# Optimization experiments

Measured on AMD Instinct MI355X. Metric: run time of the kernel, lower is better.

Reference implementation:

```python
import jax, jax.numpy as jnp
import numpy as np

B, N, M, D, R, K = 4, 4096, 4096, 256, 64, 16
EPS = 1e-5

def layernorm(x, g, b):
    m = jnp.mean(x, axis=-1, keepdims=True)
    v = jnp.var(x, axis=-1, keepdims=True)
    return (x - m) * jax.lax.rsqrt(v + EPS) * g + b

def signed_softmax(x):
    # sign(x) * softmax(|x|) along last axis
    return jnp.sign(x) * jax.nn.softmax(jnp.abs(x), axis=-1)

def unit(v):
    return v / (jnp.linalg.norm(v, axis=-1, keepdims=True) + 1e-6)

def bgather(x, idx):
    # x: [B, Msrc, ...], idx: [B, Ndst, K] -> [B, Ndst, K, ...]
    return jax.vmap(lambda xv, iv: xv[iv])(x, idx)

def topk_abs(scores, k):
    # top-k by absolute score, keep signed values
    _, idx = jax.lax.top_k(jnp.abs(scores), k)
    w = jnp.take_along_axis(scores, idx, axis=-1)
    return w, idx

def lr_bilinear_scores(src_val, dst_val, U, V):
    # scores[b, n_dst, m_src] = (dst V) . (src U) / sqrt(rank)
    sp = jnp.einsum('bmd,dr->bmr', src_val, U)
    dp = jnp.einsum('bnd,dr->bnr', dst_val, V)
    return jnp.einsum('bnr,bmr->bnm', dp, sp) / jnp.sqrt(jnp.asarray(U.shape[1], src_val.dtype))

def sparse_transition(src_state, src_val, dst_val, U, V, k):
    scores = lr_bilinear_scores(src_val, dst_val, U, V)  # [B, Ndst, Msrc]
    w, idx = topk_abs(scores, k)                          # [B, Ndst, k]
    wts = signed_softmax(w) * jax.nn.softplus(bgather(src_state, idx))
    msgs = unit(bgather(src_val, idx))                    # direction-only messages
    dval = jnp.einsum('bnk,bnkd->bnd', wts, msgs)
    dstate = jnp.sum(wts, axis=-1)
    return dstate, dval

def sparse_propagation(val_norm, U, V, k):
    scores = lr_bilinear_scores(val_norm, val_norm, U, V)  # [B, N, N]
    w, idx = topk_abs(scores, k)
    wts = signed_softmax(w)  # state_weight_edges=False
    msgs = unit(bgather(val_norm, idx))
    dval = jnp.einsum('bnk,bnkd->bnd', wts, msgs)
    dstate = jnp.sum(wts, axis=-1)
    return dstate, dval

def apply_delta(state, val, dstate, dval, g, b):
    return signed_softmax(state + dstate), layernorm(val + dval, g, b)

def setup_inputs() -> dict:
    key = jax.random.key(0)
    ks = jax.random.split(key, 12)
    std = 0.02
    return {
        'b_state': jax.random.normal(ks[0], (B, M), jnp.float32),
        'b_val': jax.random.normal(ks[1], (B, M, D), jnp.float32),
        'init_state': jax.random.normal(ks[2], (N,), jnp.float32) * std,
        'init_val': jax.random.normal(ks[3], (N, D), jnp.float32) * std,
        'U_bk': jax.random.normal(ks[4], (D, R), jnp.float32) * std,
        'V_bk': jax.random.normal(ks[5], (D, R), jnp.float32) * std,
        'U_kb': jax.random.normal(ks[6], (D, R), jnp.float32) * std,
        'V_kb': jax.random.normal(ks[7], (D, R), jnp.float32) * std,
        'U_p': jax.random.normal(ks[8], (D, R), jnp.float32) * std,
        'V_p': jax.random.normal(ks[9], (D, R), jnp.float32) * std,
        'kn_g': jnp.ones((D,), jnp.float32), 'kn_b': jnp.zeros((D,), jnp.float32),
        'bn_g': jnp.ones((D,), jnp.float32), 'bn_b': jnp.zeros((D,), jnp.float32),
        'pn_g': jnp.ones((D,), jnp.float32), 'pn_b': jnp.zeros((D,), jnp.float32),
    }

def reference(b_state, b_val, init_state, init_val, U_bk, V_bk, U_kb, V_kb, U_p, V_p, kn_g, kn_b, bn_g, bn_b, pn_g, pn_b):
    Bsz = b_state.shape[0]
    # initialize_state
    k_state = signed_softmax(jnp.broadcast_to(init_state, (Bsz, init_state.shape[0])))
    k_val = layernorm(jnp.broadcast_to(init_val, (Bsz,) + init_val.shape), kn_g, kn_b)
    # route_from_b: B -> K sparse transition, residual + k_val_norm
    nk = layernorm(k_val, kn_g, kn_b)
    ds, dv = sparse_transition(b_state, b_val, nk, U_bk, V_bk, K)
    r_state, r_val = apply_delta(k_state, k_val, ds, dv, kn_g, kn_b)
    # propagate: 1 sparse propagation layer, residual + k_val_norm
    nv = layernorm(r_val, pn_g, pn_b)
    ds, dv = sparse_propagation(nv, U_p, V_p, K)
    p_state, p_val = apply_delta(r_state, r_val, ds, dv, kn_g, kn_b)
    # transition_to_b: K -> B delta (update_b=False)
    nk2 = layernorm(p_val, kn_g, kn_b)
    nb = layernorm(b_val, bn_g, bn_b)
    bds, bdv = sparse_transition(p_state, nk2, nb, U_kb, V_kb, K)
    return (r_state, r_val, p_state, p_val, bds, bdv)
```

## Files before the change

### kernel.cpp

```cpp
#include <hip/hip_runtime.h>
#include <hip/hip_bf16.h>

#define BB 4
#define NN 4096
#define DD 256
#define RR 64
#define KK 16
#define TM 16

typedef __attribute__((ext_vector_type(8))) short bf16x8;
typedef __attribute__((ext_vector_type(4))) float f32x4;

__device__ __forceinline__ void f32_split(float x, ushort* h, ushort* l){
  __hip_bfloat16 hb = __float2bfloat16(x);
  float hf = __bfloat162float(hb);
  __hip_bfloat16 lb = __float2bfloat16(x - hf);
  *h = *(ushort*)&hb; *l = *(ushort*)&lb;
}

__global__ void __launch_bounds__(1024) ssm_kernel(
    const float* __restrict__ xf, long xf_stride,
    const float* __restrict__ add, long add_stride,
    float* __restrict__ outf, long outf_stride)
{
  __shared__ float sm[32];
  int t = threadIdx.x;
  long b = blockIdx.x;
  float x[4]; float mx = 0.f;
  #pragma unroll
  for (int j=0;j<4;j++){
    int i = t + j*1024;
    float v = xf[b*xf_stride + i];
    if (add) v += add[b*add_stride + i];
    x[j]=v; mx = fmaxf(mx, fabsf(v));
  }
  #pragma unroll
  for (int o=1;o<64;o<<=1) mx = fmaxf(mx, __shfl_xor(mx,o,64));
  int wid = t>>6;
  if ((t&63)==0) sm[wid]=mx;
  __syncthreads();
  mx = sm[0];
  #pragma unroll
  for (int w=1;w<16;w++) mx = fmaxf(mx, sm[w]);
  float e[4]; float ssum=0.f;
  #pragma unroll
  for (int j=0;j<4;j++){ e[j]=expf(fabsf(x[j])-mx); ssum+=e[j]; }
  #pragma unroll
  for (int o=1;o<64;o<<=1) ssum += __shfl_xor(ssum,o,64);
  if ((t&63)==0) sm[16+wid]=ssum;
  __syncthreads();
  ssum = sm[16];
  #pragma unroll
  for (int w=1;w<16;w++) ssum += sm[16+w];
  float inv = 1.0f/ssum;
  #pragma unroll
  for (int j=0;j<4;j++){
    int i = t + j*1024;
    float sg = (x[j]>0.f)?1.f:((x[j]<0.f)?-1.f:0.f);
    outf[b*outf_stride + i] = sg*e[j]*inv;
  }
}

__global__ void __launch_bounds__(256) proj_ln_kernel(
    const float* __restrict__ src,
    const float* __restrict__ lg, const float* __restrict__ lb, int nln,
    const float* __restrict__ U, ushort* __restrict__ oUh, ushort* __restrict__ oUl, float scaleU,
    const float* __restrict__ V, ushort* __restrict__ oVh, ushort* __restrict__ oVl, float scaleV,
    float* __restrict__ nvout, float* __restrict__ nrmout)
{
  __shared__ float xs[TM][DD];
  __shared__ float ut[64*64];
  __shared__ float vt[64*64];
  int t = threadIdx.x;
  int wid = t>>6, lane = t&63;
  long row0 = (long)blockIdx.x*TM;

  float gv[4], bv[4];
  if (nln){
    #pragma unroll
    for (int u=0;u<4;u++){ int d=u*64+lane; gv[u]=lg[d]; bv[u]=lb[d]; }
  }
  for (int rr=0; rr<4; rr++){
    int r = wid*4 + rr;
    const float* srow = src + (row0 + r)*DD;
    float x[4];
    #pragma unroll
    for (int u=0;u<4;u++) x[u] = srow[u*64 + lane];
    for (int p=0;p<nln;p++){
      float s=0.f,q=0.f;
      #pragma unroll
      for (int u=0;u<4;u++){ s+=x[u]; q+=x[u]*x[u]; }
      #pragma unroll
      for (int o=1;o<64;o<<=1){ s+=__shfl_xor(s,o,64); q+=__shfl_xor(q,o,64); }
      float m = s*(1.f/DD), var = q*(1.f/DD)-m*m, rstd = rsqrtf(var+1e-5f);
      #pragma unroll
      for (int u=0;u<4;u++) x[u] = (x[u]-m)*rstd*gv[u]+bv[u];
    }
    if (nrmout){
      float ss=0.f;
      #pragma unroll
      for (int u=0;u<4;u++) ss += x[u]*x[u];
      #pragma unroll
      for (int o=1;o<64;o<<=1) ss += __shfl_xor(ss,o,64);
      if (lane==0) nrmout[row0 + r] = 1.f/(sqrtf(ss)+1e-6f);
    }
    if (nvout){
      #pragma unroll
      for (int u=0;u<4;u++) nvout[(row0 + r)*DD + u*64 + lane] = x[u];
    }
    #pragma unroll
    for (int u=0;u<4;u++) xs[r][u*64+lane] = x[u];
  }
  __syncthreads();

  float aU[4] = {0.f,0.f,0.f,0.f};
  float aV[4] = {0.f,0.f,0.f,0.f};
  for (int kt=0; kt<4; kt++){
    const float4* Ut = (const float4*)(U + (long)kt*64*RR);
    #pragma unroll
    for (int i=0;i<4;i++) ((float4*)ut)[i*256 + t] = Ut[i*256 + t];
    if (V){
      const float4* Vt = (const float4*)(V + (long)kt*64*RR);
      #pragma unroll
      for (int i=0;i<4;i++) ((float4*)vt)[i*256 + t] = Vt[i*256 + t];
    }
    __syncthreads();
    #pragma unroll 4
    for (int dd=0; dd<64; dd+=4){
      float4 xq[4];
      #pragma unroll
      for (int r=0;r<4;r++) xq[r] = *(const float4*)&xs[wid*4+r][kt*64+dd];
      #pragma unroll
      for (int j=0;j<4;j++){
        float uv = ut[(dd+j)*64 + lane];
        float vv = V ? vt[(dd+j)*64 + lane] : 0.f;
        #pragma unroll
        for (int r=0;r<4;r++){
          float xv = (j==0)?xq[r].x:(j==1)?xq[r].y:(j==2)?xq[r].z:xq[r].w;
          aU[r] += xv*uv;
          if (V) aV[r] += xv*vv;
        }
      }
    }
    __syncthreads();
  }
  #pragma unroll
  for (int r=0;r<4;r++){
    long row = row0 + wid*4 + r;
    ushort h, l;
    f32_split(aU[r]*scaleU, &h, &l);
    oUh[row*RR + lane] = h; oUl[row*RR + lane] = l;
    if (V){
      f32_split(aV[r]*scaleV, &h, &l);
      oVh[row*RR + lane] = h; oVl[row*RR + lane] = l;
    }
  }
}

__global__ void __launch_bounds__(256) score_mfma(
    const ushort* __restrict__ dph, const ushort* __restrict__ dpl, long dp_bs,
    const ushort* __restrict__ sph, const ushort* __restrict__ spl,
    float* __restrict__ scores, int n0, int cr)
{
  int b = blockIdx.z;
  int t = threadIdx.x;
  int w = t >> 6, lane = t & 63;
  int wr = w >> 1, wc = w & 1;
  int row16 = lane & 15;
  int quad  = lane >> 4;
  long dst0 = (long)n0 + blockIdx.y*128 + wr*64;
  long src0 = (long)blockIdx.x*128 + wc*64;
  const ushort* Ah = dph + (long)b*dp_bs + (dst0 + row16)*RR + quad*8;
  const ushort* Al = dpl + (long)b*dp_bs + (dst0 + row16)*RR + quad*8;
  const ushort* Bh = sph + (long)b*NN*RR + (src0 + row16)*RR + quad*8;
  const ushort* Bl = spl + (long)b*NN*RR + (src0 + row16)*RR + quad*8;
  f32x4 acc[4][4];
  #pragma unroll
  for (int mi=0;mi<4;mi++)
    #pragma unroll
    for (int ni=0;ni<4;ni++) acc[mi][ni] = (f32x4){0.f,0.f,0.f,0.f};
  #pragma unroll
  for (int s=0; s<2; s++){
    bf16x8 ah[4], al[4], bh[4], bl[4];
    #pragma unroll
    for (int mi=0;mi<4;mi++){
      ah[mi] = *(const bf16x8*)(Ah + (long)mi*16*RR + s*32);
      al[mi] = *(const bf16x8*)(Al + (long)mi*16*RR + s*32);
    }
    #pragma unroll
    for (int ni=0;ni<4;ni++){
      bh[ni] = *(const bf16x8*)(Bh + (long)ni*16*RR + s*32);
      bl[ni] = *(const bf16x8*)(Bl + (long)ni*16*RR + s*32);
    }
    #pragma unroll
    for (int mi=0;mi<4;mi++){
      #pragma unroll
      for (int ni=0;ni<4;ni++){
        acc[mi][ni] = __builtin_amdgcn_mfma_f32_16x16x32_bf16(ah[mi], bh[ni], acc[mi][ni], 0,0,0);
        acc[mi][ni] = __builtin_amdgcn_mfma_f32_16x16x32_bf16(ah[mi], bl[ni], acc[mi][ni], 0,0,0);
        acc[mi][ni] = __builtin_amdgcn_mfma_f32_16x16x32_bf16(al[mi], bh[ni], acc[mi][ni], 0,0,0);
      }
    }
  }
  long crow0 = (long)b*cr + (dst0 - n0);
  #pragma unroll
  for (int mi=0;mi<4;mi++){
    #pragma unroll
    for (int ni=0;ni<4;ni++){
      #pragma unroll
      for (int reg=0;reg<4;reg++){
        long r = crow0 + mi*16 + quad*4 + reg;
        scores[r*NN + src0 + ni*16 + row16] = acc[mi][ni][reg];
      }
    }
  }
}

__global__ void __launch_bounds__(256) topk_kernel(
    const float* __restrict__ scores,
    float* __restrict__ wout, int* __restrict__ iout,
    int n0, int cr)
{
  __shared__ float candV[4][128];
  __shared__ int   candI[4][128];
  int wid  = threadIdx.x >> 6;
  int lane = threadIdx.x & 63;
  int g = blockIdx.x*4 + wid;
  int b = g / cr;
  int i = g - b*cr;
  const float* s = scores + ((long)b*cr + i)*NN;
  float v[64];
  #pragma unroll
  for (int q=0;q<16;q++)
    *(float4*)&v[q*4] = *(const float4*)(s + lane*64 + q*4);

  float lm = 0.f;
  #pragma unroll
  for (int j=0;j<64;j++) lm = fmaxf(lm, fabsf(v[j]));

  float cur = lm, T = 0.f;
  for (int t=0;t<16;t++){
    float m = cur;
    #pragma unroll
    for (int o=1;o<64;o<<=1) m = fmaxf(m, __shfl_xor(m,o,64));
    T = m;
    unsigned long long msk = __ballot(cur == m);
    int low = __ffsll(msk) - 1;
    if (lane == low) cur = -1.f;
  }

  int cnt = 0;
  #pragma unroll
  for (int j=0;j<64;j++) cnt += (fabsf(v[j]) >= T) ? 1 : 0;
  int xs = cnt;
  #pragma unroll
  for (int o=1;o<64;o<<=1){ int y=__shfl_up(xs,o,64); if (lane>=o) xs+=y; }
  int tot = __shfl(xs,63,64);
  bool fast = (tot <= 128);
  if (fast){
    candV[wid][lane]=0.f;        candV[wid][lane+64]=0.f;
    candI[wid][lane]=0x7fffffff; candI[wid][lane+64]=0x7fffffff;
    int p = xs - cnt;
    #pragma unroll
    for (int j=0;j<64;j++){
      if (fabsf(v[j]) >= T){ candV[wid][p]=v[j]; candI[wid][p]=lane*64+j; p++; }
    }
  }
  __syncthreads();
  long orow = ((long)b*NN + n0 + i)*KK;
  if (fast){
    float cv0=candV[wid][lane], cv1=candV[wid][lane+64];
    int   ci0=candI[wid][lane], ci1=candI[wid][lane+64];
    float k0=fabsf(cv0), k1=fabsf(cv1);
    bool f0=(ci0==0x7fffffff), f1=(ci1==0x7fffffff);
    for (int t=0;t<KK;t++){
      float bk; int bgi; float bv;
      bool pick0 = !f0 && (f1 || k0>k1 || (k0==k1 && ci0<ci1));
      if (pick0){ bk=k0; bgi=ci0; bv=cv0; }
      else if (!f1){ bk=k1; bgi=ci1; bv=cv1; }
      else { bk=-1.f; bgi=0x7fffffff; bv=0.f; }
      #pragma unroll
      for (int o=1;o<64;o<<=1){
        float ko=__shfl_xor(bk,o,64);
        int  gio=__shfl_xor(bgi,o,64);
        float vo=__shfl_xor(bv,o,64);
        if (ko>bk || (ko==bk && gio<bgi)){ bk=ko; bgi=gio; bv=vo; }
      }
      if (lane==0){ wout[orow+t]=bv; iout[orow+t]=bgi; }
      if (!f0 && bgi==ci0) f0=true;
      else if (!f1 && bgi==ci1) f1=true;
    }
  } else {
    unsigned long long cons = 0ull;
    float bk=-1.f, bval=0.f; int bj=0;
    #pragma unroll
    for (int j=0;j<64;j++){
      float k = fabsf(v[j]);
      if (k > bk){ bk=k; bj=j; bval=v[j]; }
    }
    for (int t=0;t<KK;t++){
      float k = bk; int gi = lane*64 + bj; float val = bval;
      #pragma unroll
      for (int o=1;o<64;o<<=1){
        float ko = __shfl_xor(k,o,64);
        int  gio = __shfl_xor(gi,o,64);
        float vo = __shfl_xor(val,o,64);
        if (ko > k || (ko == k && gio < gi)){ k=ko; gi=gio; val=vo; }
      }
      if (lane == 0){ wout[orow+t]=val; iout[orow+t]=gi; }
      if (lane == (gi>>6)){
        cons |= 1ull << (gi & 63);
        bk=-1.f; bj=0; bval=0.f;
        #pragma unroll
        for (int j=0;j<64;j++){
          if (!((cons>>j)&1ull)){
            float kk=fabsf(v[j]);
            if (kk>bk){ bk=kk; bj=j; bval=v[j]; }
          }
        }
      }
    }
  }
}

__global__ void __launch_bounds__(256) gather_kernel(
    const float* __restrict__ wbuf, const int* __restrict__ ibuf,
    const float* __restrict__ sv, long sv_bs,
    const float* __restrict__ nrm,
    const float* __restrict__ st, long st_bs,
    const float* __restrict__ base, int base_mod,
    const float* __restrict__ bg, const float* __restrict__ bb,
    const float* __restrict__ og, const float* __restrict__ ob,
    float* __restrict__ outv, float* __restrict__ ds)
{
  int t = threadIdx.x;
  int wid = t>>6, lane = t&63;
  long row = (long)blockIdx.x*4 + wid;
  int b = (int)(row >> 12);

  int kk = lane & 15;
  int si = ibuf[row*KK + kk];
  float w = wbuf[row*KK + kk];
  float aw = fabsf(w);
  float m = aw;
  #pragma unroll
  for (int o=1;o<16;o<<=1) m = fmaxf(m, __shfl_xor(m,o,64));
  float e = expf(aw - m);
  float Z = e;
  #pragma unroll
  for (int o=1;o<16;o<<=1) Z += __shfl_xor(Z,o,64);
  float sg = (w>0.f)?1.f:((w<0.f)?-1.f:0.f);
  float vv = sg*e/Z;
  if (st){
    float stv = st[(long)b*st_bs + si];
    vv *= fmaxf(stv,0.f) + log1pf(expf(-fabsf(stv)));
  }
  float wsum = vv;
  #pragma unroll
  for (int o=1;o<16;o<<=1) wsum += __shfl_xor(wsum,o,64);
  if (lane==0) ds[row] = wsum;
  float wkp = vv * nrm[(long)b*NN + si];

  float4 acc = {0.f,0.f,0.f,0.f};
  const float* svb = sv + (long)b*sv_bs;
  #pragma unroll
  for (int k=0;k<KK;k++){
    int   sik = __shfl(si, k, 64);
    float wk  = __shfl(wkp, k, 64);
    float4 mq = *(const float4*)(svb + (long)sik*DD + lane*4);
    acc.x += wk*mq.x; acc.y += wk*mq.y; acc.z += wk*mq.z; acc.w += wk*mq.w;
  }

  if (!base){
    *(float4*)(outv + row*DD + lane*4) = acc;
    return;
  }
  const float* brow = base + (long)(base_mod ? (row % base_mod) : row)*DD;
  float4 x4 = *(const float4*)(brow + lane*4);
  if (bg){
    float s = x4.x+x4.y+x4.z+x4.w;
    float q = x4.x*x4.x+x4.y*x4.y+x4.z*x4.z+x4.w*x4.w;
    #pragma unroll
    for (int o=1;o<64;o<<=1){ s+=__shfl_xor(s,o,64); q+=__shfl_xor(q,o,64); }
    float mm=s*(1.f/DD), var=q*(1.f/DD)-mm*mm, rstd=rsqrtf(var+1e-5f);
    float4 g4 = *(const float4*)(bg + lane*4);
    float4 b4 = *(const float4*)(bb + lane*4);
    x4.x=(x4.x-mm)*rstd*g4.x+b4.x; x4.y=(x4.y-mm)*rstd*g4.y+b4.y;
    x4.z=(x4.z-mm)*rstd*g4.z+b4.z; x4.w=(x4.w-mm)*rstd*g4.w+b4.w;
  }
  x4.x+=acc.x; x4.y+=acc.y; x4.z+=acc.z; x4.w+=acc.w;
  {
    float s = x4.x+x4.y+x4.z+x4.w;
    float q = x4.x*x4.x+x4.y*x4.y+x4.z*x4.z+x4.w*x4.w;
    #pragma unroll
    for (int o=1;o<64;o<<=1){ s+=__shfl_xor(s,o,64); q+=__shfl_xor(q,o,64); }
    float mm=s*(1.f/DD), var=q*(1.f/DD)-mm*mm, rstd=rsqrtf(var+1e-5f);
    float4 g4 = *(const float4*)(og + lane*4);
    float4 b4 = *(const float4*)(ob + lane*4);
    float4 o4;
    o4.x=(x4.x-mm)*rstd*g4.x+b4.x; o4.y=(x4.y-mm)*rstd*g4.y+b4.y;
    o4.z=(x4.z-mm)*rstd*g4.z+b4.z; o4.w=(x4.w-mm)*rstd*g4.w+b4.w;
    *(float4*)(outv + row*DD + lane*4) = o4;
  }
}

extern "C" void kernel_launch(void* const* d_in, const int* in_sizes, int n_in,
                              void* d_out, int out_size, void* d_ws, size_t ws_size,
                              hipStream_t stream)
{
  const float* b_state    = (const float*)d_in[0];
  const float* b_val      = (const float*)d_in[1];
  const float* init_state = (const float*)d_in[2];
  const float* init_val   = (const float*)d_in[3];
  const float* U_bk = (const float*)d_in[4];
  const float* V_bk = (const float*)d_in[5];
  const float* U_kb = (const float*)d_in[6];
  const float* V_kb = (const float*)d_in[7];
  const float* U_p  = (const float*)d_in[8];
  const float* V_p  = (const float*)d_in[9];
  const float* kn_g = (const float*)d_in[10];
  const float* kn_b = (const float*)d_in[11];
  const float* bn_g = (const float*)d_in[12];
  const float* bn_b = (const float*)d_in[13];
  const float* pn_g = (const float*)d_in[14];
  const float* pn_b = (const float*)d_in[15];
  float* out = (float*)d_out;

  const long o_rstate = 0;
  const long o_rval   = (long)BB*NN;
  const long o_pstate = o_rval + (long)BB*NN*DD;
  const long o_pval   = o_pstate + (long)BB*NN;
  const long o_bds    = o_pval + (long)BB*NN*DD;
  const long o_bdv    = o_bds + (long)BB*NN;

  float* RVAL = out + o_rval;
  float* PVAL = out + o_pval;
  float* RST  = out + o_rstate;
  float* PST  = out + o_pstate;

  ushort* SPh = (ushort*)d_ws;
  ushort* SPl = SPh + (long)BB*NN*RR;
  ushort* DPh = SPl + (long)BB*NN*RR;
  ushort* DPl = DPh + (long)BB*NN*RR;
  float* WB   = (float*)(DPl + (long)BB*NN*RR);
  int*   IB   = (int*)(WB + (long)BB*NN*KK);
  float* KST  = (float*)(IB + (long)BB*NN*KK);
  float* DS   = KST + NN;
  float* NV   = DS + (long)BB*NN;
  float* NRM  = NV + (long)BB*NN*DD;
  float* SC   = NRM + (long)BB*NN;
  long fixed_bytes = (char*)SC - (char*)d_ws;
  int cr = 2048;
  while (cr > 128 && fixed_bytes + (long)BB*cr*NN*4 > (long)ws_size) cr >>= 1;

  auto run_scores = [&](const ushort* dh, const ushort* dl, long dpbs,
                        const ushort* sh, const ushort* sl){
    int nch = NN / cr;
    for (int c=0;c<nch;c++){
      score_mfma<<<dim3(NN/128, cr/128, BB), 256, 0, stream>>>(dh, dl, dpbs, sh, sl, SC, c*cr, cr);
      topk_kernel<<<dim3(BB*cr/4), 256, 0, stream>>>(SC, WB, IB, c*cr, cr);
    }
  };

  ssm_kernel<<<1,1024,0,stream>>>(init_state, 0, nullptr, 0, KST, 0);

  proj_ln_kernel<<<NN/TM,256,0,stream>>>(init_val, kn_g, kn_b, 2,
                                         V_bk, DPh, DPl, 0.125f, nullptr, nullptr, nullptr, 0.f,
                                         nullptr, nullptr);
  proj_ln_kernel<<<BB*NN/TM,256,0,stream>>>(b_val, nullptr, nullptr, 0,
                                            U_bk, SPh, SPl, 1.0f, nullptr, nullptr, nullptr, 0.f,
                                            nullptr, NRM);
  run_scores(DPh, DPl, 0, SPh, SPl);
  gather_kernel<<<BB*NN/4,256,0,stream>>>(WB, IB,
      b_val, (long)NN*DD, NRM,
      b_state, (long)NN,
      init_val, NN, kn_g, kn_b, kn_g, kn_b,
      RVAL, DS);
  ssm_kernel<<<BB,1024,0,stream>>>(KST, 0, DS, NN, RST, NN);

  proj_ln_kernel<<<BB*NN/TM,256,0,stream>>>(RVAL, pn_g, pn_b, 1,
                                            U_p, SPh, SPl, 1.0f, V_p, DPh, DPl, 0.125f,
                                            NV, NRM);
  run_scores(DPh, DPl, (long)NN*RR, SPh, SPl);
  gather_kernel<<<BB*NN/4,256,0,stream>>>(WB, IB,
      NV, (long)NN*DD, NRM,
      nullptr, 0,
      RVAL, 0, nullptr, nullptr, kn_g, kn_b,
      PVAL, DS);
  ssm_kernel<<<BB,1024,0,stream>>>(RST, NN, DS, NN, PST, NN);

  proj_ln_kernel<<<BB*NN/TM,256,0,stream>>>(PVAL, kn_g, kn_b, 1,
                                            U_kb, SPh, SPl, 1.0f, nullptr, nullptr, nullptr, 0.f,
                                            NV, NRM);
  proj_ln_kernel<<<BB*NN/TM,256,0,stream>>>(b_val, bn_g, bn_b, 1,
                                            V_kb, DPh, DPl, 0.125f, nullptr, nullptr, nullptr, 0.f,
                                            nullptr, nullptr);
  run_scores(DPh, DPl, (long)NN*RR, SPh, SPl);
  gather_kernel<<<BB*NN/4,256,0,stream>>>(WB, IB,
      NV, (long)NN*DD, NRM,
      PST, (long)NN,
      nullptr, 0, nullptr, nullptr, nullptr, nullptr,
      out + o_bdv, out + o_bds);
}
```

Before: 891.3 us.

## Replace materialized score matrix with two-pass recompute threshold top-k selection

```diff
diff --git a/kernel.cpp b/kernel.cpp
--- a/kernel.cpp
+++ b/kernel.cpp
@@ -16,6 +16,10 @@
   float hf = __bfloat162float(hb);
   __hip_bfloat16 lb = __float2bfloat16(x - hf);
   *h = *(ushort*)&hb; *l = *(ushort*)&lb;
+}
+
+__device__ __forceinline__ float bf2f(ushort u){
+  unsigned x = ((unsigned)u)<<16; return __builtin_bit_cast(float, x);
 }
 
 __global__ void __launch_bounds__(1024) ssm_kernel(
@@ -157,120 +161,169 @@
   }
 }
 
-__global__ void __launch_bounds__(256) score_mfma(
+
+#define SPLITS 4
+#define STEPS  (NN/SPLITS/16)
+#define CCAP   128
+
+#define LOADA(AH0,AH1,AL0,AL1, STEP) { \
+    const ushort* p_ = Sh + (long)(STEP)*16*RR; \
+    const ushort* q_ = Sl + (long)(STEP)*16*RR; \
+    AH0 = *(const bf16x8*)(p_);      AH1 = *(const bf16x8*)(p_ + 32); \
+    AL0 = *(const bf16x8*)(q_);      AL1 = *(const bf16x8*)(q_ + 32); }
+
+#define MFMA6(AH0,AH1,AL0,AL1, ACC) { \
+    ACC = __builtin_amdgcn_mfma_f32_16x16x32_bf16(AH0, dh0, ACC, 0,0,0); \
+    ACC = __builtin_amdgcn_mfma_f32_16x16x32_bf16(AL0, dh0, ACC, 0,0,0); \
+    ACC = __builtin_amdgcn_mfma_f32_16x16x32_bf16(AH0, dl0, ACC, 0,0,0); \
+    ACC = __builtin_amdgcn_mfma_f32_16x16x32_bf16(AH1, dh1, ACC, 0,0,0); \
+    ACC = __builtin_amdgcn_mfma_f32_16x16x32_bf16(AL1, dh1, ACC, 0,0,0); \
+    ACC = __builtin_amdgcn_mfma_f32_16x16x32_bf16(AH1, dl1, ACC, 0,0,0); }
+
+__global__ void __launch_bounds__(256) score_max(
     const ushort* __restrict__ dph, const ushort* __restrict__ dpl, long dp_bs,
     const ushort* __restrict__ sph, const ushort* __restrict__ spl,
-    float* __restrict__ scores, int n0, int cr)
-{
-  int b = blockIdx.z;
-  int t = threadIdx.x;
-  int w = t >> 6, lane = t & 63;
-  int wr = w >> 1, wc = w & 1;
-  int row16 = lane & 15;
-  int quad  = lane >> 4;
-  long dst0 = (long)n0 + blockIdx.y*128 + wr*64;
-  long src0 = (long)blockIdx.x*128 + wc*64;
-  const ushort* Ah = dph + (long)b*dp_bs + (dst0 + row16)*RR + quad*8;
-  const ushort* Al = dpl + (long)b*dp_bs + (dst0 + row16)*RR + quad*8;
-  const ushort* Bh = sph + (long)b*NN*RR + (src0 + row16)*RR + quad*8;
-  const ushort* Bl = spl + (long)b*NN*RR + (src0 + row16)*RR + quad*8;
-  f32x4 acc[4][4];
-  #pragma unroll
-  for (int mi=0;mi<4;mi++)
-    #pragma unroll
-    for (int ni=0;ni<4;ni++) acc[mi][ni] = (f32x4){0.f,0.f,0.f,0.f};
-  #pragma unroll
-  for (int s=0; s<2; s++){
-    bf16x8 ah[4], al[4], bh[4], bl[4];
-    #pragma unroll
-    for (int mi=0;mi<4;mi++){
-      ah[mi] = *(const bf16x8*)(Ah + (long)mi*16*RR + s*32);
-      al[mi] = *(const bf16x8*)(Al + (long)mi*16*RR + s*32);
-    }
-    #pragma unroll
-    for (int ni=0;ni<4;ni++){
-      bh[ni] = *(const bf16x8*)(Bh + (long)ni*16*RR + s*32);
-      bl[ni] = *(const bf16x8*)(Bl + (long)ni*16*RR + s*32);
-    }
-    #pragma unroll
-    for (int mi=0;mi<4;mi++){
-      #pragma unroll
-      for (int ni=0;ni<4;ni++){
-        acc[mi][ni] = __builtin_amdgcn_mfma_f32_16x16x32_bf16(ah[mi], bh[ni], acc[mi][ni], 0,0,0);
-        acc[mi][ni] = __builtin_amdgcn_mfma_f32_16x16x32_bf16(ah[mi], bl[ni], acc[mi][ni], 0,0,0);
-        acc[mi][ni] = __builtin_amdgcn_mfma_f32_16x16x32_bf16(al[mi], bh[ni], acc[mi][ni], 0,0,0);
-      }
-    }
-  }
-  long crow0 = (long)b*cr + (dst0 - n0);
-  #pragma unroll
-  for (int mi=0;mi<4;mi++){
-    #pragma unroll
-    for (int ni=0;ni<4;ni++){
-      #pragma unroll
-      for (int reg=0;reg<4;reg++){
-        long r = crow0 + mi*16 + quad*4 + reg;
-        scores[r*NN + src0 + ni*16 + row16] = acc[mi][ni][reg];
-      }
-    }
-  }
-}
-
-__global__ void __launch_bounds__(256) topk_kernel(
-    const float* __restrict__ scores,
-    float* __restrict__ wout, int* __restrict__ iout,
-    int n0, int cr)
-{
-  __shared__ float candV[4][128];
-  __shared__ int   candI[4][128];
-  int wid  = threadIdx.x >> 6;
-  int lane = threadIdx.x & 63;
-  int g = blockIdx.x*4 + wid;
-  int b = g / cr;
-  int i = g - b*cr;
-  const float* s = scores + ((long)b*cr + i)*NN;
-  float v[64];
-  #pragma unroll
-  for (int q=0;q<16;q++)
-    *(float4*)&v[q*4] = *(const float4*)(s + lane*64 + q*4);
-
-  float lm = 0.f;
-  #pragma unroll
-  for (int j=0;j<64;j++) lm = fmaxf(lm, fabsf(v[j]));
-
-  float cur = lm, T = 0.f;
+    float* __restrict__ PM)
+{
+  const int b = blockIdx.z, split = blockIdx.y;
+  const int t = threadIdx.x;
+  const int w = t>>6, lane = t&63;
+  const int r16 = lane&15, quad = lane>>4;
+  const int dst = blockIdx.x*64 + w*16 + r16;
+  const int src0 = split*(NN/SPLITS);
+
+  const ushort* Dh = dph + (long)b*dp_bs + (long)dst*RR + quad*8;
+  const ushort* Dl = dpl + (long)b*dp_bs + (long)dst*RR + quad*8;
+  bf16x8 dh0 = *(const bf16x8*)(Dh);
+  bf16x8 dh1 = *(const bf16x8*)(Dh + 32);
+  bf16x8 dl0 = *(const bf16x8*)(Dl);
+  bf16x8 dl1 = *(const bf16x8*)(Dl + 32);
+
+  const ushort* Sh = sph + (long)b*NN*RR + (long)(src0 + r16)*RR + quad*8;
+  const ushort* Sl = spl + (long)b*NN*RR + (long)(src0 + r16)*RR + quad*8;
+
+  float pm0=0.f, pm1=0.f, pm2=0.f, pm3=0.f;
+  bf16x8 xh0,xh1,xl0,xl1, yh0,yh1,yl0,yl1;
+  LOADA(xh0,xh1,xl0,xl1, 0)
+  for (int st=0; st<STEPS; st+=2){
+    LOADA(yh0,yh1,yl0,yl1, st+1)
+    {
+      f32x4 acc = (f32x4){0.f,0.f,0.f,0.f};
+      MFMA6(xh0,xh1,xl0,xl1, acc)
+      pm0 = fmaxf(pm0, fabsf(acc[0])); pm1 = fmaxf(pm1, fabsf(acc[1]));
+      pm2 = fmaxf(pm2, fabsf(acc[2])); pm3 = fmaxf(pm3, fabsf(acc[3]));
+    }
+    if (st+2 < STEPS) LOADA(xh0,xh1,xl0,xl1, st+2)
+    {
+      f32x4 acc = (f32x4){0.f,0.f,0.f,0.f};
+      MFMA6(yh0,yh1,yl0,yl1, acc)
+      pm0 = fmaxf(pm0, fabsf(acc[0])); pm1 = fmaxf(pm1, fabsf(acc[1]));
+      pm2 = fmaxf(pm2, fabsf(acc[2])); pm3 = fmaxf(pm3, fabsf(acc[3]));
+    }
+  }
+  float* pmr = PM + ((long)b*NN + dst)*64 + split*16 + quad*4;
+  pmr[0]=pm0; pmr[1]=pm1; pmr[2]=pm2; pmr[3]=pm3;
+}
+
+__global__ void __launch_bounds__(256) tsel_kernel(
+    const float* __restrict__ PM, float* __restrict__ T, int* __restrict__ CNT)
+{
+  int wid = threadIdx.x>>6, lane = threadIdx.x&63;
+  long g = (long)blockIdx.x*4 + wid;
+  float cur = PM[g*64 + lane];
+  float Tv = 0.f;
   for (int t=0;t<16;t++){
     float m = cur;
     #pragma unroll
     for (int o=1;o<64;o<<=1) m = fmaxf(m, __shfl_xor(m,o,64));
-    T = m;
+    Tv = m;
     unsigned long long msk = __ballot(cur == m);
     int low = __ffsll(msk) - 1;
     if (lane == low) cur = -1.f;
   }
-
-  int cnt = 0;
-  #pragma unroll
-  for (int j=0;j<64;j++) cnt += (fabsf(v[j]) >= T) ? 1 : 0;
-  int xs = cnt;
-  #pragma unroll
-  for (int o=1;o<64;o<<=1){ int y=__shfl_up(xs,o,64); if (lane>=o) xs+=y; }
-  int tot = __shfl(xs,63,64);
-  bool fast = (tot <= 128);
-  if (fast){
-    candV[wid][lane]=0.f;        candV[wid][lane+64]=0.f;
-    candI[wid][lane]=0x7fffffff; candI[wid][lane+64]=0x7fffffff;
-    int p = xs - cnt;
-    #pragma unroll
-    for (int j=0;j<64;j++){
-      if (fabsf(v[j]) >= T){ candV[wid][p]=v[j]; candI[wid][p]=lane*64+j; p++; }
-    }
-  }
-  __syncthreads();
-  long orow = ((long)b*NN + n0 + i)*KK;
-  if (fast){
-    float cv0=candV[wid][lane], cv1=candV[wid][lane+64];
-    int   ci0=candI[wid][lane], ci1=candI[wid][lane+64];
+  if (lane==0){ T[g] = Tv; CNT[g] = 0; }
+}
+
+__global__ void __launch_bounds__(256) score_collect(
+    const ushort* __restrict__ dph, const ushort* __restrict__ dpl, long dp_bs,
+    const ushort* __restrict__ sph, const ushort* __restrict__ spl,
+    const float* __restrict__ T, int* __restrict__ CNT,
+    float* __restrict__ CV, int* __restrict__ CI)
+{
+  const int b = blockIdx.z, split = blockIdx.y;
+  const int t = threadIdx.x;
+  const int w = t>>6, lane = t&63;
+  const int r16 = lane&15, quad = lane>>4;
+  const int dst = blockIdx.x*64 + w*16 + r16;
+  const int src0 = split*(NN/SPLITS);
+  const long row = (long)b*NN + dst;
+
+  const ushort* Dh = dph + (long)b*dp_bs + (long)dst*RR + quad*8;
+  const ushort* Dl = dpl + (long)b*dp_bs + (long)dst*RR + quad*8;
+  bf16x8 dh0 = *(const bf16x8*)(Dh);
+  bf16x8 dh1 = *(const bf16x8*)(Dh + 32);
+  bf16x8 dl0 = *(const bf16x8*)(Dl);
+  bf16x8 dl1 = *(const bf16x8*)(Dl + 32);
+
+  const ushort* Sh = sph + (long)b*NN*RR + (long)(src0 + r16)*RR + quad*8;
+  const ushort* Sl = spl + (long)b*NN*RR + (long)(src0 + r16)*RR + quad*8;
+
+  const float Trow = T[row];
+  int* cntp = CNT + row;
+  float* cvp = CV + row*CCAP;
+  int*   cip = CI + row*CCAP;
+
+#define COLLECT(ACC, STEP) { \
+    float m01 = fmaxf(fabsf(ACC[0]), fabsf(ACC[1])); \
+    float m23 = fmaxf(fabsf(ACC[2]), fabsf(ACC[3])); \
+    if (fmaxf(m01,m23) >= Trow){ \
+      int sbase = src0 + (STEP)*16 + quad*4; \
+      _Pragma("unroll") \
+      for (int r=0;r<4;r++){ \
+        if (fabsf(ACC[r]) >= Trow){ \
+          int slot = atomicAdd(cntp, 1); \
+          if (slot < CCAP){ cvp[slot] = ACC[r]; cip[slot] = sbase + r; } \
+        } \
+      } \
+    } }
+
+  bf16x8 xh0,xh1,xl0,xl1, yh0,yh1,yl0,yl1;
+  LOADA(xh0,xh1,xl0,xl1, 0)
+  for (int st=0; st<STEPS; st+=2){
+    LOADA(yh0,yh1,yl0,yl1, st+1)
+    {
+      f32x4 acc = (f32x4){0.f,0.f,0.f,0.f};
+      MFMA6(xh0,xh1,xl0,xl1, acc)
+      COLLECT(acc, st)
+    }
+    if (st+2 < STEPS) LOADA(xh0,xh1,xl0,xl1, st+2)
+    {
+      f32x4 acc = (f32x4){0.f,0.f,0.f,0.f};
+      MFMA6(yh0,yh1,yl0,yl1, acc)
+      COLLECT(acc, st+1)
+    }
+  }
+#undef COLLECT
+}
+
+__global__ void __launch_bounds__(256) sel16_kernel(
+    const float* __restrict__ CV, const int* __restrict__ CI, const int* __restrict__ CNT,
+    const ushort* __restrict__ dph, const ushort* __restrict__ dpl, long dp_bs,
+    const ushort* __restrict__ sph, const ushort* __restrict__ spl,
+    float* __restrict__ wout, int* __restrict__ iout)
+{
+  int wid = threadIdx.x>>6, lane = threadIdx.x&63;
+  long g = (long)blockIdx.x*4 + wid;
+  int b = (int)(g >> 12);
+  int n = (int)(g & (NN-1));
+  int C = CNT[g];
+  long orow = g*KK;
+  if (C <= CCAP){
+    const float* cvp = CV + g*CCAP;
+    const int*   cip = CI + g*CCAP;
+    float cv0 = 0.f, cv1 = 0.f; int ci0 = 0x7fffffff, ci1 = 0x7fffffff;
+    if (lane < C){ cv0 = cvp[lane]; ci0 = cip[lane]; }
+    if (lane+64 < C){ cv1 = cvp[lane+64]; ci1 = cip[lane+64]; }
     float k0=fabsf(cv0), k1=fabsf(cv1);
     bool f0=(ci0==0x7fffffff), f1=(ci1==0x7fffffff);
     for (int t=0;t<KK;t++){
@@ -291,6 +344,23 @@
       else if (!f1 && bgi==ci1) f1=true;
     }
   } else {
+    const ushort* dh = dph + (long)b*dp_bs + (long)n*RR;
+    const ushort* dl = dpl + (long)b*dp_bs + (long)n*RR;
+    const ushort* shb = sph + (long)b*NN*RR;
+    const ushort* slb = spl + (long)b*NN*RR;
+    float v[64];
+    for (int j=0;j<64;j++){
+      int src = lane*64 + j;
+      const ushort* sh = shb + (long)src*RR;
+      const ushort* sl = slb + (long)src*RR;
+      float acc = 0.f;
+      for (int k=0;k<RR;k++){
+        float d = bf2f(dh[k]) + bf2f(dl[k]);
+        float s = bf2f(sh[k]) + bf2f(sl[k]);
+        acc += d*s;
+      }
+      v[j] = acc;
+    }
     unsigned long long cons = 0ull;
     float bk=-1.f, bval=0.f; int bj=0;
     #pragma unroll
@@ -448,18 +518,17 @@
   float* DS   = KST + NN;
   float* NV   = DS + (long)BB*NN;
   float* NRM  = NV + (long)BB*NN*DD;
-  float* SC   = NRM + (long)BB*NN;
-  long fixed_bytes = (char*)SC - (char*)d_ws;
-  int cr = 2048;
-  while (cr > 128 && fixed_bytes + (long)BB*cr*NN*4 > (long)ws_size) cr >>= 1;
-
-  auto run_scores = [&](const ushort* dh, const ushort* dl, long dpbs,
-                        const ushort* sh, const ushort* sl){
-    int nch = NN / cr;
-    for (int c=0;c<nch;c++){
-      score_mfma<<<dim3(NN/128, cr/128, BB), 256, 0, stream>>>(dh, dl, dpbs, sh, sl, SC, c*cr, cr);
-      topk_kernel<<<dim3(BB*cr/4), 256, 0, stream>>>(SC, WB, IB, c*cr, cr);
-    }
+  float* PM   = NRM + (long)BB*NN;
+  float* TT   = PM + (long)BB*NN*64;
+  int*   CNT  = (int*)(TT + (long)BB*NN);
+  float* CV   = (float*)(CNT + (long)BB*NN);
+  int*   CI   = (int*)(CV + (long)BB*NN*CCAP);
+
+  auto run_scores = [&](long dpbs){
+    score_max<<<dim3(NN/64, SPLITS, BB), 256, 0, stream>>>(DPh, DPl, dpbs, SPh, SPl, PM);
+    tsel_kernel<<<BB*NN/4, 256, 0, stream>>>(PM, TT, CNT);
+    score_collect<<<dim3(NN/64, SPLITS, BB), 256, 0, stream>>>(DPh, DPl, dpbs, SPh, SPl, TT, CNT, CV, CI);
+    sel16_kernel<<<BB*NN/4, 256, 0, stream>>>(CV, CI, CNT, DPh, DPl, dpbs, SPh, SPl, WB, IB);
   };
 
   ssm_kernel<<<1,1024,0,stream>>>(init_state, 0, nullptr, 0, KST, 0);
@@ -470,7 +539,7 @@
   proj_ln_kernel<<<BB*NN/TM,256,0,stream>>>(b_val, nullptr, nullptr, 0,
                                             U_bk, SPh, SPl, 1.0f, nullptr, nullptr, nullptr, 0.f,
                                             nullptr, NRM);
-  run_scores(DPh, DPl, 0, SPh, SPl);
+  run_scores(0);
   gather_kernel<<<BB*NN/4,256,0,stream>>>(WB, IB,
       b_val, (long)NN*DD, NRM,
       b_state, (long)NN,
@@ -481,7 +550,7 @@
   proj_ln_kernel<<<BB*NN/TM,256,0,stream>>>(RVAL, pn_g, pn_b, 1,
                                             U_p, SPh, SPl, 1.0f, V_p, DPh, DPl, 0.125f,
                                             NV, NRM);
-  run_scores(DPh, DPl, (long)NN*RR, SPh, SPl);
+  run_scores((long)NN*RR);
   gather_kernel<<<BB*NN/4,256,0,stream>>>(WB, IB,
       NV, (long)NN*DD, NRM,
       nullptr, 0,
@@ -495,7 +564,7 @@
   proj_ln_kernel<<<BB*NN/TM,256,0,stream>>>(b_val, bn_g, bn_b, 1,
                                             V_kb, DPh, DPl, 0.125f, nullptr, nullptr, nullptr, 0.f,
                                             nullptr, nullptr);
-  run_scores(DPh, DPl, (long)NN*RR, SPh, SPl);
+  run_scores((long)NN*RR);
   gather_kernel<<<BB*NN/4,256,0,stream>>>(WB, IB,
       NV, (long)NN*DD, NRM,
       PST, (long)NN,
```

Measured after the change: 1.300 ms. 1.46x slower.

## Split top-k rows across four waves with merge; template projection on V presence

Applied to the files above, without the earlier changes.

```diff
diff --git a/kernel.cpp b/kernel.cpp
--- a/kernel.cpp
+++ b/kernel.cpp
@@ -61,6 +61,7 @@
   }
 }
 
+template<int HASV>
 __global__ void __launch_bounds__(256) proj_ln_kernel(
     const float* __restrict__ src,
     const float* __restrict__ lg, const float* __restrict__ lb, int nln,
@@ -70,7 +71,7 @@
 {
   __shared__ float xs[TM][DD];
   __shared__ float ut[64*64];
-  __shared__ float vt[64*64];
+  __shared__ float vt[HASV ? 64*64 : 4];
   int t = threadIdx.x;
   int wid = t>>6, lane = t&63;
   long row0 = (long)blockIdx.x*TM;
@@ -119,7 +120,7 @@
     const float4* Ut = (const float4*)(U + (long)kt*64*RR);
     #pragma unroll
     for (int i=0;i<4;i++) ((float4*)ut)[i*256 + t] = Ut[i*256 + t];
-    if (V){
+    if (HASV){
       const float4* Vt = (const float4*)(V + (long)kt*64*RR);
       #pragma unroll
       for (int i=0;i<4;i++) ((float4*)vt)[i*256 + t] = Vt[i*256 + t];
@@ -133,12 +134,12 @@
       #pragma unroll
       for (int j=0;j<4;j++){
         float uv = ut[(dd+j)*64 + lane];
-        float vv = V ? vt[(dd+j)*64 + lane] : 0.f;
+        float vv = HASV ? vt[(dd+j)*64 + lane] : 0.f;
         #pragma unroll
         for (int r=0;r<4;r++){
           float xv = (j==0)?xq[r].x:(j==1)?xq[r].y:(j==2)?xq[r].z:xq[r].w;
           aU[r] += xv*uv;
-          if (V) aV[r] += xv*vv;
+          if (HASV) aV[r] += xv*vv;
         }
       }
     }
@@ -150,7 +151,7 @@
     ushort h, l;
     f32_split(aU[r]*scaleU, &h, &l);
     oUh[row*RR + lane] = h; oUl[row*RR + lane] = l;
-    if (V){
+    if (HASV){
       f32_split(aV[r]*scaleV, &h, &l);
       oVh[row*RR + lane] = h; oVl[row*RR + lane] = l;
     }
@@ -223,20 +224,22 @@
 {
   __shared__ float candV[4][128];
   __shared__ int   candI[4][128];
-  int wid  = threadIdx.x >> 6;
+  __shared__ float pV[4][16];
+  __shared__ int   pI[4][16];
+  int w    = threadIdx.x >> 6;
   int lane = threadIdx.x & 63;
-  int g = blockIdx.x*4 + wid;
+  int g = blockIdx.x;
   int b = g / cr;
   int i = g - b*cr;
-  const float* s = scores + ((long)b*cr + i)*NN;
-  float v[64];
-  #pragma unroll
-  for (int q=0;q<16;q++)
-    *(float4*)&v[q*4] = *(const float4*)(s + lane*64 + q*4);
+  const float* s = scores + ((long)b*cr + i)*NN + w*1024;
+  float v[16];
+  #pragma unroll
+  for (int q=0;q<4;q++)
+    *(float4*)&v[q*4] = *(const float4*)(s + lane*16 + q*4);
 
   float lm = 0.f;
   #pragma unroll
-  for (int j=0;j<64;j++) lm = fmaxf(lm, fabsf(v[j]));
+  for (int j=0;j<16;j++) lm = fmaxf(lm, fabsf(v[j]));
 
   float cur = lm, T = 0.f;
   for (int t=0;t<16;t++){
@@ -251,26 +254,25 @@
 
   int cnt = 0;
   #pragma unroll
-  for (int j=0;j<64;j++) cnt += (fabsf(v[j]) >= T) ? 1 : 0;
+  for (int j=0;j<16;j++) cnt += (fabsf(v[j]) >= T) ? 1 : 0;
   int xs = cnt;
   #pragma unroll
   for (int o=1;o<64;o<<=1){ int y=__shfl_up(xs,o,64); if (lane>=o) xs+=y; }
   int tot = __shfl(xs,63,64);
   bool fast = (tot <= 128);
   if (fast){
-    candV[wid][lane]=0.f;        candV[wid][lane+64]=0.f;
-    candI[wid][lane]=0x7fffffff; candI[wid][lane+64]=0x7fffffff;
+    candV[w][lane]=0.f;        candV[w][lane+64]=0.f;
+    candI[w][lane]=0x7fffffff; candI[w][lane+64]=0x7fffffff;
     int p = xs - cnt;
     #pragma unroll
-    for (int j=0;j<64;j++){
-      if (fabsf(v[j]) >= T){ candV[wid][p]=v[j]; candI[wid][p]=lane*64+j; p++; }
+    for (int j=0;j<16;j++){
+      if (fabsf(v[j]) >= T){ candV[w][p]=v[j]; candI[w][p]=w*1024 + lane*16 + j; p++; }
     }
   }
   __syncthreads();
-  long orow = ((long)b*NN + n0 + i)*KK;
   if (fast){
-    float cv0=candV[wid][lane], cv1=candV[wid][lane+64];
-    int   ci0=candI[wid][lane], ci1=candI[wid][lane+64];
+    float cv0=candV[w][lane], cv1=candV[w][lane+64];
+    int   ci0=candI[w][lane], ci1=candI[w][lane+64];
     float k0=fabsf(cv0), k1=fabsf(cv1);
     bool f0=(ci0==0x7fffffff), f1=(ci1==0x7fffffff);
     for (int t=0;t<KK;t++){
@@ -286,20 +288,20 @@
         float vo=__shfl_xor(bv,o,64);
         if (ko>bk || (ko==bk && gio<bgi)){ bk=ko; bgi=gio; bv=vo; }
       }
-      if (lane==0){ wout[orow+t]=bv; iout[orow+t]=bgi; }
+      if (lane==0){ pV[w][t]=bv; pI[w][t]=bgi; }
       if (!f0 && bgi==ci0) f0=true;
       else if (!f1 && bgi==ci1) f1=true;
     }
   } else {
-    unsigned long long cons = 0ull;
+    unsigned int cons = 0;
     float bk=-1.f, bval=0.f; int bj=0;
     #pragma unroll
-    for (int j=0;j<64;j++){
+    for (int j=0;j<16;j++){
       float k = fabsf(v[j]);
       if (k > bk){ bk=k; bj=j; bval=v[j]; }
     }
     for (int t=0;t<KK;t++){
-      float k = bk; int gi = lane*64 + bj; float val = bval;
+      float k = bk; int gi = w*1024 + lane*16 + bj; float val = bval;
       #pragma unroll
       for (int o=1;o<64;o<<=1){
         float ko = __shfl_xor(k,o,64);
@@ -307,18 +309,41 @@
         float vo = __shfl_xor(val,o,64);
         if (ko > k || (ko == k && gio < gi)){ k=ko; gi=gio; val=vo; }
       }
-      if (lane == 0){ wout[orow+t]=val; iout[orow+t]=gi; }
-      if (lane == (gi>>6)){
-        cons |= 1ull << (gi & 63);
+      if (lane == 0){ pV[w][t]=val; pI[w][t]=gi; }
+      int rel = gi - w*1024;
+      if (lane == (rel>>4)){
+        cons |= 1u << (rel & 15);
         bk=-1.f; bj=0; bval=0.f;
         #pragma unroll
-        for (int j=0;j<64;j++){
-          if (!((cons>>j)&1ull)){
+        for (int j=0;j<16;j++){
+          if (!((cons>>j)&1u)){
             float kk=fabsf(v[j]);
             if (kk>bk){ bk=kk; bj=j; bval=v[j]; }
           }
         }
       }
+    }
+  }
+  __syncthreads();
+  if (threadIdx.x < 64){
+    int s4 = lane & 3;
+    long orow = ((long)b*NN + n0 + i)*KK;
+    int ptr = 0;
+    for (int r=0;r<KK;r++){
+      float hv = 0.f, hk = -1.f; int hi_ = 0x7fffffff;
+      if (ptr < 16){
+        hv = pV[s4][ptr]; hi_ = pI[s4][ptr]; hk = fabsf(hv);
+      }
+      float bk=hk, bv=hv; int bi=hi_;
+      #pragma unroll
+      for (int o=1;o<4;o<<=1){
+        float ko=__shfl_xor(bk,o,64);
+        int   io=__shfl_xor(bi,o,64);
+        float vo=__shfl_xor(bv,o,64);
+        if (ko>bk || (ko==bk && io<bi)){ bk=ko; bi=io; bv=vo; }
+      }
+      if (threadIdx.x==0){ wout[orow+r]=bv; iout[orow+r]=bi; }
+      if (bi == hi_) ptr++;
     }
   }
 }
@@ -458,18 +483,18 @@
     int nch = NN / cr;
     for (int c=0;c<nch;c++){
       score_mfma<<<dim3(NN/128, cr/128, BB), 256, 0, stream>>>(dh, dl, dpbs, sh, sl, SC, c*cr, cr);
-      topk_kernel<<<dim3(BB*cr/4), 256, 0, stream>>>(SC, WB, IB, c*cr, cr);
+      topk_kernel<<<dim3(BB*cr), 256, 0, stream>>>(SC, WB, IB, c*cr, cr);
     }
   };
 
   ssm_kernel<<<1,1024,0,stream>>>(init_state, 0, nullptr, 0, KST, 0);
 
-  proj_ln_kernel<<<NN/TM,256,0,stream>>>(init_val, kn_g, kn_b, 2,
-                                         V_bk, DPh, DPl, 0.125f, nullptr, nullptr, nullptr, 0.f,
-                                         nullptr, nullptr);
-  proj_ln_kernel<<<BB*NN/TM,256,0,stream>>>(b_val, nullptr, nullptr, 0,
-                                            U_bk, SPh, SPl, 1.0f, nullptr, nullptr, nullptr, 0.f,
-                                            nullptr, NRM);
+  proj_ln_kernel<0><<<NN/TM,256,0,stream>>>(init_val, kn_g, kn_b, 2,
+                                            V_bk, DPh, DPl, 0.125f, nullptr, nullptr, nullptr, 0.f,
+                                            nullptr, nullptr);
+  proj_ln_kernel<0><<<BB*NN/TM,256,0,stream>>>(b_val, nullptr, nullptr, 0,
+                                               U_bk, SPh, SPl, 1.0f, nullptr, nullptr, nullptr, 0.f,
+                                               nullptr, NRM);
   run_scores(DPh, DPl, 0, SPh, SPl);
   gather_kernel<<<BB*NN/4,256,0,stream>>>(WB, IB,
       b_val, (long)NN*DD, NRM,
@@ -478,9 +503,9 @@
       RVAL, DS);
   ssm_kernel<<<BB,1024,0,stream>>>(KST, 0, DS, NN, RST, NN);
 
-  proj_ln_kernel<<<BB*NN/TM,256,0,stream>>>(RVAL, pn_g, pn_b, 1,
-                                            U_p, SPh, SPl, 1.0f, V_p, DPh, DPl, 0.125f,
-                                            NV, NRM);
+  proj_ln_kernel<1><<<BB*NN/TM,256,0,stream>>>(RVAL, pn_g, pn_b, 1,
+                                               U_p, SPh, SPl, 1.0f, V_p, DPh, DPl, 0.125f,
+                                               NV, NRM);
   run_scores(DPh, DPl, (long)NN*RR, SPh, SPl);
   gather_kernel<<<BB*NN/4,256,0,stream>>>(WB, IB,
       NV, (long)NN*DD, NRM,
@@ -489,12 +514,12 @@
       PVAL, DS);
   ssm_kernel<<<BB,1024,0,stream>>>(RST, NN, DS, NN, PST, NN);
 
-  proj_ln_kernel<<<BB*NN/TM,256,0,stream>>>(PVAL, kn_g, kn_b, 1,
-                                            U_kb, SPh, SPl, 1.0f, nullptr, nullptr, nullptr, 0.f,
-                                            NV, NRM);
-  proj_ln_kernel<<<BB*NN/TM,256,0,stream>>>(b_val, bn_g, bn_b, 1,
-                                            V_kb, DPh, DPl, 0.125f, nullptr, nullptr, nullptr, 0.f,
-                                            nullptr, nullptr);
+  proj_ln_kernel<0><<<BB*NN/TM,256,0,stream>>>(PVAL, kn_g, kn_b, 1,
+                                               U_kb, SPh, SPl, 1.0f, nullptr, nullptr, nullptr, 0.f,
+                                               NV, NRM);
+  proj_ln_kernel<0><<<BB*NN/TM,256,0,stream>>>(b_val, bn_g, bn_b, 1,
+                                               V_kb, DPh, DPl, 0.125f, nullptr, nullptr, nullptr, 0.f,
+                                               nullptr, nullptr);
   run_scores(DPh, DPl, (long)NN*RR, SPh, SPl);
   gather_kernel<<<BB*NN/4,256,0,stream>>>(WB, IB,
       NV, (long)NN*DD, NRM,
```

After: 1.479 ms. 1.66x slower.
